# Kernel tuning notes

Hardware: AMD Instinct MI355X
Metric: run time of the kernel (lower is better)

## Reference

```python
import jax, jax.numpy as jnp
import numpy as np
import math

B, T, C = 8, 1024, 1024
H = 16
D = C // H
TI = 256
FF = 4 * C
EPS = 1e-5


def _ln(x, g, b):
    mu = jnp.mean(x, axis=-1, keepdims=True)
    var = jnp.mean(jnp.square(x - mu), axis=-1, keepdims=True)
    return (x - mu) * jax.lax.rsqrt(var + EPS) * g + b


def _gelu_tanh(x):
    return jax.nn.gelu(x, approximate=True)


def setup_inputs() -> dict:
    key = jax.random.key(0)
    ks = jax.random.split(key, 16)
    s = 0.02
    inp = {
        'x': jax.random.normal(ks[0], (B, T, C), jnp.float32),
        'x_img_feats': jax.random.normal(ks[1], (B, TI, C), jnp.float32),
        'ln1_g': jnp.ones((C,), jnp.float32), 'ln1_b': jnp.zeros((C,), jnp.float32),
        'ln2_g': jnp.ones((C,), jnp.float32), 'ln2_b': jnp.zeros((C,), jnp.float32),
        'W_attn': jax.random.normal(ks[2], (C, 3 * C), jnp.float32) * s,
        'b_attn': jnp.zeros((3 * C,), jnp.float32),
        'W_aproj': jax.random.normal(ks[3], (C, C), jnp.float32) * s,
        'b_aproj': jnp.zeros((C,), jnp.float32),
        'Wq': jax.random.normal(ks[4], (C, C), jnp.float32) * s,
        'bq': jnp.zeros((C,), jnp.float32),
        'Wk': jax.random.normal(ks[5], (C, C), jnp.float32) * s,
        'bk': jnp.zeros((C,), jnp.float32),
        'Wv': jax.random.normal(ks[6], (C, C), jnp.float32) * s,
        'bv': jnp.zeros((C,), jnp.float32),
        'Wcproj': jax.random.normal(ks[7], (C, C), jnp.float32) * s,
        'bcproj': jnp.zeros((C,), jnp.float32),
        'W_fc': jax.random.normal(ks[8], (C, FF), jnp.float32) * s,
        'b_fc': jnp.zeros((FF,), jnp.float32),
        'W_mproj': jax.random.normal(ks[9], (FF, C), jnp.float32) * s,
        'b_mproj': jnp.zeros((C,), jnp.float32),
    }
    return inp


def _heads(t):
    # (B, S, C) -> (B, H, S, D)
    return t.reshape(t.shape[0], t.shape[1], H, D).transpose(0, 2, 1, 3)


def _merge(t):
    # (B, H, S, D) -> (B, S, C)
    return t.transpose(0, 2, 1, 3).reshape(t.shape[0], t.shape[2], C)


def reference(x, x_img_feats, ln1_g, ln1_b, ln2_g, ln2_b,
              W_attn, b_attn, W_aproj, b_aproj,
              Wq, bq, Wk, bk, Wv, bv, Wcproj, bcproj,
              W_fc, b_fc, W_mproj, b_mproj):
    scale = 1.0 / math.sqrt(D)

    # causal self-attention
    h = _ln(x, ln1_g, ln1_b)
    qkv = h @ W_attn + b_attn
    q, k, v = jnp.split(qkv, 3, axis=-1)
    q, k, v = _heads(q), _heads(k), _heads(v)
    att = jnp.einsum('bhtd,bhsd->bhts', q, k) * scale
    causal = jnp.tril(jnp.ones((T, T), bool))
    att = jnp.where(causal[None, None], att, -jnp.inf)
    att = jax.nn.softmax(att, axis=-1)
    sa = _merge(jnp.einsum('bhts,bhsd->bhtd', att, v)) @ W_aproj + b_aproj
    x = x + sa

    # cross-attention (text queries, image keys/values)
    ht = _ln(x, ln1_g, ln1_b)
    q = _heads(ht @ Wq + bq)
    k = _heads(x_img_feats @ Wk + bk)
    v = _heads(x_img_feats @ Wv + bv)
    catt = jax.nn.softmax(jnp.einsum('bhtd,bhsd->bhts', q, k) * scale, axis=-1)
    ca = _merge(jnp.einsum('bhts,bhsd->bhtd', catt, v)) @ Wcproj + bcproj
    x = x + ca

    # MLP
    h2 = _ln(x, ln2_g, ln2_b)
    x = x + _gelu_tanh(h2 @ W_fc + b_fc) @ W_mproj + b_mproj
    return x
```

## Files before the change

kernel.cpp:

```cpp
#include <hip/hip_runtime.h>

#define B_ 8
#define T_ 1024
#define C_ 1024
#define H_ 16
#define D_ 64
#define TI_ 256
#define FF_ 4096
#define BT_ (B_*T_)
#define BTI_ (B_*TI_)

typedef __bf16 bf16x8 __attribute__((ext_vector_type(8)));
typedef float f32x4 __attribute__((ext_vector_type(4)));
typedef float f32x16 __attribute__((ext_vector_type(16)));

__device__ __forceinline__ unsigned short f2bf(float f){
  unsigned u = __float_as_uint(f);
  u += 0x7fffu + ((u>>16)&1u);
  return (unsigned short)(u>>16);
}

__device__ __forceinline__ void cp16(const void* g, void* l){
  __builtin_amdgcn_global_load_lds(
      (const __attribute__((address_space(1))) unsigned int*)(unsigned long long)g,
      (__attribute__((address_space(3))) unsigned int*)(unsigned long long)l,
      16, 0, 0);
}

__global__ __launch_bounds__(256) void gemm_bt(
    const unsigned short* __restrict__ A,
    const unsigned short* __restrict__ Bt,
    const float* __restrict__ bias,
    const float* __restrict__ resid,
    void* __restrict__ outp,
    int M, int N, int K, int mode)
{
  __shared__ unsigned short sA[128*64];
  __shared__ unsigned short sB[128*64];
  const int tid  = threadIdx.x;
  const int wid  = tid >> 6;
  const int lane = tid & 63;
  const int l32  = lane & 31;
  const int khalf = lane >> 5;

  int lin = blockIdx.y * gridDim.x + blockIdx.x;
  int nb  = gridDim.x * gridDim.y;
  if ((nb & 7) == 0){
    int per = nb >> 3;
    lin = (lin >> 3) + (lin & 7) * per;
  }
  const int bx = lin % gridDim.x;
  const int by = lin / gridDim.x;
  const int row0 = by * 128;
  const int col0 = bx * 128;
  const int wr = (wid >> 1) * 64;
  const int wc = (wid & 1) * 64;

  f32x16 acc[2][2];
#pragma unroll
  for (int i=0;i<2;i++)
#pragma unroll
    for (int j=0;j<2;j++)
#pragma unroll
      for (int r=0;r<16;r++) acc[i][j][r] = 0.f;

  for (int k0 = 0; k0 < K; k0 += 64){
    if (k0) __syncthreads();
#pragma unroll
    for (int r=0;r<8;r++){
      int chunk = wid*8 + r;
      int cA = chunk & 15;
      int slot = cA*64 + lane;
      int row = slot >> 3;
      int cc = (slot & 7) ^ (row & 7);
      if (chunk < 16)
        cp16(A  + (size_t)(row0+row)*K + (k0 + cc*8), sA + cA*512);
      else
        cp16(Bt + (size_t)(col0+row)*K + (k0 + cc*8), sB + cA*512);
    }
    __syncthreads();
    const char* sAb = (const char*)sA;
    const char* sBb = (const char*)sB;
#pragma unroll
    for (int kk=0;kk<4;kk++){
      bf16x8 af[2], bfb[2];
#pragma unroll
      for (int i=0;i<2;i++){
        int rr = wr + i*32 + l32;
        af[i] = *(const bf16x8*)(sAb + rr*128 + ((((kk<<1)+khalf) ^ (rr&7))<<4));
      }
#pragma unroll
      for (int j=0;j<2;j++){
        int rr = wc + j*32 + l32;
        bfb[j] = *(const bf16x8*)(sBb + rr*128 + ((((kk<<1)+khalf) ^ (rr&7))<<4));
      }
#pragma unroll
      for (int i=0;i<2;i++)
#pragma unroll
        for (int j=0;j<2;j++)
          acc[i][j] = __builtin_amdgcn_mfma_f32_32x32x16_bf16(af[i], bfb[j], acc[i][j], 0, 0, 0);
    }
  }

#pragma unroll
  for (int j=0;j<2;j++){
    int gc = col0 + wc + j*32 + l32;
    float bz = bias[gc];
#pragma unroll
    for (int i=0;i<2;i++){
      int gr_base = row0 + wr + i*32 + 4*khalf;
#pragma unroll
      for (int reg=0; reg<16; ++reg){
        int gr = gr_base + (reg&3) + 8*(reg>>2);
        float v = acc[i][j][reg] + bz;
        size_t idx = (size_t)gr*N + gc;
        if (mode == 0){
          ((unsigned short*)outp)[idx] = f2bf(v);
        } else if (mode == 1){
          float w = 1.5957691216057308f*(v + 0.044715f*v*v*v);
          float g = v / (1.f + __expf(-w));
          ((unsigned short*)outp)[idx] = f2bf(g);
        } else {
          ((float*)outp)[idx] = resid[idx] + v;
        }
      }
    }
  }
}

__global__ __launch_bounds__(256) void ln_fwd(
    const float* __restrict__ x, const float* __restrict__ g,
    const float* __restrict__ b, unsigned short* __restrict__ out)
{
  int row = blockIdx.x, t = threadIdx.x;
  const float4* xv = (const float4*)(x + (size_t)row*C_);
  float4 v = xv[t];
  float s  = v.x+v.y+v.z+v.w;
  float ss = v.x*v.x + v.y*v.y + v.z*v.z + v.w*v.w;
#pragma unroll
  for (int o=32;o>0;o>>=1){ s += __shfl_down(s,o); ss += __shfl_down(ss,o); }
  __shared__ float red[16];
  int wid = t>>6, lane = t&63;
  if (lane==0){ red[wid]=s; red[8+wid]=ss; }
  __syncthreads();
  if (t==0){
    red[0] = red[0]+red[1]+red[2]+red[3];
    red[8] = red[8]+red[9]+red[10]+red[11];
  }
  __syncthreads();
  float mu  = red[0] * (1.f/C_);
  float var = red[8] * (1.f/C_) - mu*mu;
  float rstd = rsqrtf(var + 1e-5f);
  float4 gv = ((const float4*)g)[t];
  float4 bv = ((const float4*)b)[t];
  ushort4 o;
  o.x = f2bf((v.x-mu)*rstd*gv.x + bv.x);
  o.y = f2bf((v.y-mu)*rstd*gv.y + bv.y);
  o.z = f2bf((v.z-mu)*rstd*gv.z + bv.z);
  o.w = f2bf((v.w-mu)*rstd*gv.w + bv.w);
  ((ushort4*)(out + (size_t)row*C_))[t] = o;
}

__global__ void wconv_t(const float* __restrict__ W, unsigned short* __restrict__ Wt,
                        int Kd, int Nd)
{
  __shared__ float tile[32][33];
  int tx = threadIdx.x, ty = threadIdx.y;
  int n0 = blockIdx.x*32, k0 = blockIdx.y*32;
#pragma unroll
  for (int j=0;j<4;j++)
    tile[ty+8*j][tx] = W[(size_t)(k0+ty+8*j)*Nd + (n0+tx)];
  __syncthreads();
#pragma unroll
  for (int j=0;j<4;j++)
    Wt[(size_t)(n0+ty+8*j)*Kd + (k0+tx)] = f2bf(tile[tx][ty+8*j]);
}

__global__ void conv_bf16(const float* __restrict__ X, unsigned short* __restrict__ Y, int n4)
{
  int i = blockIdx.x*256 + threadIdx.x;
  if (i < n4){
    float4 v = ((const float4*)X)[i];
    ushort4 o; o.x=f2bf(v.x); o.y=f2bf(v.y); o.z=f2bf(v.z); o.w=f2bf(v.w);
    ((ushort4*)Y)[i] = o;
  }
}

__global__ __launch_bounds__(256) void attn_fwd(
    const unsigned short* __restrict__ Q, int ldq,
    const unsigned short* __restrict__ Kp, const unsigned short* __restrict__ Vp, int ldkv,
    int kvT, int Skv, int Tq, int causal,
    unsigned short* __restrict__ Out, int ldo, float scale)
{
  __shared__ unsigned short sK[64*64];
  __shared__ unsigned short sV[64*64];
  __shared__ unsigned short sP[4*16*64];
  const int tid = threadIdx.x;
  const int wid = tid >> 6;
  const int lane = tid & 63;
  const int quad = lane >> 4;
  const int l16 = lane & 15;
  const int qt = blockIdx.x, h = blockIdx.y, b = blockIdx.z;
  const int hoff = h * D_;

  const int qrow = qt*64 + wid*16 + l16;
  const unsigned short* qb = Q + (size_t)(b*Tq + qrow)*ldq + hoff;
  bf16x8 qf[2];
  qf[0] = *(const bf16x8*)(qb + quad*8);
  qf[1] = *(const bf16x8*)(qb + 32 + quad*8);

  f32x4 zero = {0.f,0.f,0.f,0.f};
  f32x4 O[4];
#pragma unroll
  for (int j=0;j<4;j++) O[j] = zero;
  float mrun[4], lrun[4];
#pragma unroll
  for (int r=0;r<4;r++){ mrun[r] = -1e30f; lrun[r] = 0.f; }

  const int nkb = causal ? (qt+1) : ((Skv+63)>>6);
  char* sPw = (char*)sP + wid*2048;

  for (int kb=0; kb<nkb; ++kb){
    if (kb) __syncthreads();
#pragma unroll
    for (int ss=0; ss<2; ++ss){
      int slot = tid + ss*256;
      int srow = slot >> 3;
      int cc = (slot & 7) ^ (srow & 7);
      const unsigned short* g = Kp + (size_t)(b*kvT + kb*64 + srow)*ldkv + hoff + cc*8;
      *(uint4*)((char*)sK + slot*16) = *(const uint4*)g;
    }
    {
      int s_ = lane;
      int dbase = wid*16;
      const unsigned short* gv = Vp + (size_t)(b*kvT + kb*64 + s_)*ldkv + hoff + dbase;
      unsigned short vals[16];
      *(uint4*)(vals)   = *(const uint4*)(gv);
      *(uint4*)(vals+8) = *(const uint4*)(gv+8);
      int chunk = s_ >> 3;
      int sb = (s_ & 7)*2;
#pragma unroll
      for (int jj=0; jj<16; ++jj){
        int d = dbase + jj;
        *(unsigned short*)((char*)sV + d*128 + ((chunk ^ (d&7))<<4) + sb) = vals[jj];
      }
    }
    __syncthreads();

    f32x4 sacc[4];
#pragma unroll
    for (int j=0;j<4;j++) sacc[j] = zero;
#pragma unroll
    for (int j=0;j<4;j++){
      int krow = j*16 + l16;
#pragma unroll
      for (int kk=0;kk<2;kk++){
        bf16x8 kf = *(const bf16x8*)((const char*)sK + krow*128 + (((kk*4+quad) ^ (krow&7))<<4));
        sacc[j] = __builtin_amdgcn_mfma_f32_16x16x32_bf16(qf[kk], kf, sacc[j], 0, 0, 0);
      }
    }
    const int qa0 = qt*64 + wid*16 + quad*4;
    float sc[4][4];
#pragma unroll
    for (int j=0;j<4;j++){
      int key = kb*64 + j*16 + l16;
#pragma unroll
      for (int r=0;r<4;r++){
        float v = sacc[j][r] * scale;
        if (causal && key > qa0 + r) v = -1e30f;
        sc[j][r] = v;
      }
    }
    float mnew[4], alpha[4], rs[4];
#pragma unroll
    for (int r=0;r<4;r++){
      float m = fmaxf(fmaxf(sc[0][r], sc[1][r]), fmaxf(sc[2][r], sc[3][r]));
#pragma unroll
      for (int msk=1; msk<16; msk<<=1) m = fmaxf(m, __shfl_xor(m, msk));
      mnew[r] = fmaxf(mrun[r], m);
      alpha[r] = __expf(mrun[r] - mnew[r]);
      mrun[r] = mnew[r];
      rs[r] = 0.f;
    }
#pragma unroll
    for (int j=0;j<4;j++){
#pragma unroll
      for (int r=0;r<4;r++){
        float p = __expf(sc[j][r] - mnew[r]);
        rs[r] += p;
        int prow = quad*4 + r;
        int cole = j*16 + l16;
        *(unsigned short*)(sPw + prow*128 + (((cole>>3) ^ (prow&7))<<4) + (cole&7)*2) = f2bf(p);
      }
    }
#pragma unroll
    for (int r=0;r<4;r++){
#pragma unroll
      for (int msk=1; msk<16; msk<<=1) rs[r] += __shfl_xor(rs[r], msk);
      lrun[r] = lrun[r]*alpha[r] + rs[r];
    }
#pragma unroll
    for (int j=0;j<4;j++){
      O[j][0] *= alpha[0]; O[j][1] *= alpha[1];
      O[j][2] *= alpha[2]; O[j][3] *= alpha[3];
    }
    bf16x8 pf[2];
#pragma unroll
    for (int kk=0;kk<2;kk++)
      pf[kk] = *(const bf16x8*)(sPw + l16*128 + (((kk*4+quad) ^ (l16&7))<<4));
#pragma unroll
    for (int j=0;j<4;j++){
      int vrow = j*16 + l16;
#pragma unroll
      for (int kk=0;kk<2;kk++){
        bf16x8 vf = *(const bf16x8*)((const char*)sV + vrow*128 + (((kk*4+quad) ^ (vrow&7))<<4));
        O[j] = __builtin_amdgcn_mfma_f32_16x16x32_bf16(pf[kk], vf, O[j], 0, 0, 0);
      }
    }
  }
#pragma unroll
  for (int j=0;j<4;j++){
#pragma unroll
    for (int r=0;r<4;r++){
      int qa = qt*64 + wid*16 + quad*4 + r;
      float o = O[j][r] / lrun[r];
      Out[(size_t)(b*Tq + qa)*ldo + hoff + j*16 + l16] = f2bf(o);
    }
  }
}

extern "C" void kernel_launch(void* const* d_in, const int* in_sizes, int n_in,
                              void* d_out, int out_size, void* d_ws, size_t ws_size,
                              hipStream_t stream)
{
  const float* x       = (const float*)d_in[0];
  const float* ximg    = (const float*)d_in[1];
  const float* ln1_g   = (const float*)d_in[2];
  const float* ln1_b   = (const float*)d_in[3];
  const float* ln2_g   = (const float*)d_in[4];
  const float* ln2_b   = (const float*)d_in[5];
  const float* W_attn  = (const float*)d_in[6];
  const float* b_attn  = (const float*)d_in[7];
  const float* W_aproj = (const float*)d_in[8];
  const float* b_aproj = (const float*)d_in[9];
  const float* Wq = (const float*)d_in[10];
  const float* bq = (const float*)d_in[11];
  const float* Wk = (const float*)d_in[12];
  const float* bk = (const float*)d_in[13];
  const float* Wv = (const float*)d_in[14];
  const float* bv = (const float*)d_in[15];
  const float* Wcproj  = (const float*)d_in[16];
  const float* bcproj  = (const float*)d_in[17];
  const float* W_fc    = (const float*)d_in[18];
  const float* b_fc    = (const float*)d_in[19];
  const float* W_mproj = (const float*)d_in[20];
  const float* b_mproj = (const float*)d_in[21];

  char* ws = (char*)d_ws;
  unsigned short* wt_attn  = (unsigned short*)(ws + 0);
  unsigned short* wt_aproj = (unsigned short*)(ws + 6291456);
  unsigned short* wt_q     = (unsigned short*)(ws + 8388608);
  unsigned short* wt_k     = (unsigned short*)(ws + 10485760);
  unsigned short* wt_v     = (unsigned short*)(ws + 12582912);
  unsigned short* wt_cproj = (unsigned short*)(ws + 14680064);
  unsigned short* wt_fc    = (unsigned short*)(ws + 16777216);
  unsigned short* wt_mproj = (unsigned short*)(ws + 25165824);
  unsigned short* ximg_bf  = (unsigned short*)(ws + 33554432);
  float*          xcur     = (float*)(ws + 37748736);
  unsigned short* h_bf     = (unsigned short*)(ws + 71303168);
  unsigned short* qkv      = (unsigned short*)(ws + 88080384);
  unsigned short* att_out  = (unsigned short*)(ws + 88080384 + 50331648);
  unsigned short* u_bf     = (unsigned short*)(ws + 88080384);
  unsigned short* q2   = (unsigned short*)(ws + 155189248);
  unsigned short* k2v2 = (unsigned short*)(ws + 171966464);
  unsigned short* ca   = (unsigned short*)(ws + 180355072);
  float*          bkv  = (float*)(ws + 197132288);

  dim3 tb(32,8);
  wconv_t<<<dim3(96,32),  tb, 0, stream>>>(W_attn,  wt_attn,  1024, 3072);
  wconv_t<<<dim3(32,32),  tb, 0, stream>>>(W_aproj, wt_aproj, 1024, 1024);
  wconv_t<<<dim3(32,32),  tb, 0, stream>>>(Wq,      wt_q,     1024, 1024);
  wconv_t<<<dim3(32,32),  tb, 0, stream>>>(Wk,      wt_k,     1024, 1024);
  wconv_t<<<dim3(32,32),  tb, 0, stream>>>(Wv,      wt_v,     1024, 1024);
  wconv_t<<<dim3(32,32),  tb, 0, stream>>>(Wcproj,  wt_cproj, 1024, 1024);
  wconv_t<<<dim3(128,32), tb, 0, stream>>>(W_fc,    wt_fc,    1024, 4096);
  wconv_t<<<dim3(32,128), tb, 0, stream>>>(W_mproj, wt_mproj, 4096, 1024);
  conv_bf16<<<BTI_*C_/4/256, 256, 0, stream>>>(ximg, ximg_bf, BTI_*C_/4);
  hipMemcpyAsync(xcur, x, (size_t)BT_*C_*4, hipMemcpyDeviceToDevice, stream);
  hipMemcpyAsync(bkv,        bk, 4096, hipMemcpyDeviceToDevice, stream);
  hipMemcpyAsync(bkv + 1024, bv, 4096, hipMemcpyDeviceToDevice, stream);

  ln_fwd<<<BT_, 256, 0, stream>>>(x, ln1_g, ln1_b, h_bf);
  gemm_bt<<<dim3(24,64), 256, 0, stream>>>(h_bf, wt_attn, b_attn, nullptr, qkv, BT_, 3072, 1024, 0);
  attn_fwd<<<dim3(16,H_,B_), 256, 0, stream>>>(qkv, 3072, qkv+1024, qkv+2048, 3072,
                                               T_, T_, T_, 1, att_out, C_, 0.125f);
  gemm_bt<<<dim3(8,64), 256, 0, stream>>>(att_out, wt_aproj, b_aproj, xcur, xcur, BT_, 1024, 1024, 2);

  ln_fwd<<<BT_, 256, 0, stream>>>(xcur, ln1_g, ln1_b, h_bf);
  gemm_bt<<<dim3(8,64), 256, 0, stream>>>(h_bf, wt_q, bq, nullptr, q2, BT_, 1024, 1024, 0);
  gemm_bt<<<dim3(16,16), 256, 0, stream>>>(ximg_bf, wt_k, bkv, nullptr, k2v2, BTI_, 2048, 1024, 0);
  attn_fwd<<<dim3(16,H_,B_), 256, 0, stream>>>(q2, 1024, k2v2, k2v2+1024, 2048,
                                               TI_, TI_, T_, 0, ca, C_, 0.125f);
  gemm_bt<<<dim3(8,64), 256, 0, stream>>>(ca, wt_cproj, bcproj, xcur, xcur, BT_, 1024, 1024, 2);

  ln_fwd<<<BT_, 256, 0, stream>>>(xcur, ln2_g, ln2_b, h_bf);
  gemm_bt<<<dim3(32,64), 256, 0, stream>>>(h_bf, wt_fc, b_fc, nullptr, u_bf, BT_, 4096, 1024, 1);
  gemm_bt<<<dim3(8,64), 256, 0, stream>>>(u_bf, wt_mproj, b_mproj, xcur, (float*)d_out, BT_, 1024, 4096, 2);
}
```

Before: 839.2 us.

## Double-buffer attention K/V tiles, process two query tiles per block, batch weight conversions

The attention kernel now handles 128 query rows per block as two 64-row sub-tiles that share each loaded K/V tile, halving K/V traffic per query. It double-buffers K (via async global-to-LDS copies) and V (via register prefetch) so loads overlap the MFMA work. It also schedules heavy causal tiles first, folds the softmax scale into exp2, and sets a 3-blocks-per-CU launch bound. Separately, the five 1024x1024 weight conversions are merged into one launch, and the GEMM's XCD-aware block remapping is removed, which may hurt L2 locality on the GEMMs.

```diff
diff --git a/kernel.cpp b/kernel.cpp
--- a/kernel.cpp
+++ b/kernel.cpp
@@ -43,16 +43,8 @@
   const int l32  = lane & 31;
   const int khalf = lane >> 5;
 
-  int lin = blockIdx.y * gridDim.x + blockIdx.x;
-  int nb  = gridDim.x * gridDim.y;
-  if ((nb & 7) == 0){
-    int per = nb >> 3;
-    lin = (lin >> 3) + (lin & 7) * per;
-  }
-  const int bx = lin % gridDim.x;
-  const int by = lin / gridDim.x;
-  const int row0 = by * 128;
-  const int col0 = bx * 128;
+  const int row0 = blockIdx.y * 128;
+  const int col0 = blockIdx.x * 128;
   const int wr = (wid >> 1) * 64;
   const int wc = (wid & 1) * 64;
 
@@ -176,6 +168,27 @@
     Wt[(size_t)(n0+ty+8*j)*Kd + (k0+tx)] = f2bf(tile[tx][ty+8*j]);
 }
 
+__global__ void wconv_t5(const float* W0, const float* W1, const float* W2,
+                         const float* W3, const float* W4,
+                         unsigned short* O0, unsigned short* O1, unsigned short* O2,
+                         unsigned short* O3, unsigned short* O4)
+{
+  __shared__ float tile[32][33];
+  const float* Ws[5] = {W0,W1,W2,W3,W4};
+  unsigned short* Os[5] = {O0,O1,O2,O3,O4};
+  const float* W = Ws[blockIdx.z];
+  unsigned short* Wt = Os[blockIdx.z];
+  int tx = threadIdx.x, ty = threadIdx.y;
+  int n0 = blockIdx.x*32, k0 = blockIdx.y*32;
+#pragma unroll
+  for (int j=0;j<4;j++)
+    tile[ty+8*j][tx] = W[(size_t)(k0+ty+8*j)*1024 + (n0+tx)];
+  __syncthreads();
+#pragma unroll
+  for (int j=0;j<4;j++)
+    Wt[(size_t)(n0+ty+8*j)*1024 + (k0+tx)] = f2bf(tile[tx][ty+8*j]);
+}
+
 __global__ void conv_bf16(const float* __restrict__ X, unsigned short* __restrict__ Y, int n4)
 {
   int i = blockIdx.x*256 + threadIdx.x;
@@ -186,145 +199,193 @@
   }
 }
 
-__global__ __launch_bounds__(256) void attn_fwd(
+__global__ __launch_bounds__(256,3) void attn_fwd(
     const unsigned short* __restrict__ Q, int ldq,
     const unsigned short* __restrict__ Kp, const unsigned short* __restrict__ Vp, int ldkv,
     int kvT, int Skv, int Tq, int causal,
     unsigned short* __restrict__ Out, int ldo, float scale)
 {
-  __shared__ unsigned short sK[64*64];
-  __shared__ unsigned short sV[64*64];
-  __shared__ unsigned short sP[4*16*64];
+  __shared__ unsigned short sK[2][64*64];
+  __shared__ unsigned short sVT[2][64*64];
+  __shared__ unsigned short sP[8*16*64];
   const int tid = threadIdx.x;
   const int wid = tid >> 6;
   const int lane = tid & 63;
   const int quad = lane >> 4;
   const int l16 = lane & 15;
-  const int qt = blockIdx.x, h = blockIdx.y, b = blockIdx.z;
+  const int qt = gridDim.x - 1 - blockIdx.x;
+  const int h = blockIdx.y, b = blockIdx.z;
   const int hoff = h * D_;
-
-  const int qrow = qt*64 + wid*16 + l16;
-  const unsigned short* qb = Q + (size_t)(b*Tq + qrow)*ldq + hoff;
-  bf16x8 qf[2];
-  qf[0] = *(const bf16x8*)(qb + quad*8);
-  qf[1] = *(const bf16x8*)(qb + 32 + quad*8);
-
-  f32x4 zero = {0.f,0.f,0.f,0.f};
-  f32x4 O[4];
-#pragma unroll
-  for (int j=0;j<4;j++) O[j] = zero;
-  float mrun[4], lrun[4];
-#pragma unroll
-  for (int r=0;r<4;r++){ mrun[r] = -1e30f; lrun[r] = 0.f; }
-
-  const int nkb = causal ? (qt+1) : ((Skv+63)>>6);
-  char* sPw = (char*)sP + wid*2048;
-
-  for (int kb=0; kb<nkb; ++kb){
-    if (kb) __syncthreads();
+  const float c2 = scale * 1.4426950408889634f;
+
+  bf16x8 qf[2][2];
+#pragma unroll
+  for (int s=0;s<2;s++){
+    int qrow = qt*128 + s*64 + wid*16 + l16;
+    const unsigned short* qb = Q + (size_t)(b*Tq + qrow)*ldq + hoff;
+    qf[s][0] = *(const bf16x8*)(qb + quad*8);
+    qf[s][1] = *(const bf16x8*)(qb + 32 + quad*8);
+  }
+
+  f32x4 O[2][4];
+#pragma unroll
+  for (int s=0;s<2;s++)
+#pragma unroll
+    for (int j=0;j<4;j++) O[s][j] = (f32x4){0.f,0.f,0.f,0.f};
+  float mrun[2][4], lrun[2][4];
+#pragma unroll
+  for (int s=0;s<2;s++)
+#pragma unroll
+    for (int r=0;r<4;r++){ mrun[s][r] = -1e30f; lrun[s][r] = 0.f; }
+
+  const int nkb = causal ? (2*qt + 2) : ((Skv + 63) >> 6);
+
+  uint4 vreg0, vreg1;
+  const int vsrow = lane;
+  const int vdbase = wid*16;
+
+  {
+    const unsigned short* gv = Vp + (size_t)(b*kvT + vsrow)*ldkv + hoff + vdbase;
+    vreg0 = *(const uint4*)gv; vreg1 = *(const uint4*)(gv+8);
 #pragma unroll
     for (int ss=0; ss<2; ++ss){
       int slot = tid + ss*256;
       int srow = slot >> 3;
       int cc = (slot & 7) ^ (srow & 7);
-      const unsigned short* g = Kp + (size_t)(b*kvT + kb*64 + srow)*ldkv + hoff + cc*8;
-      *(uint4*)((char*)sK + slot*16) = *(const uint4*)g;
-    }
-    {
-      int s_ = lane;
-      int dbase = wid*16;
-      const unsigned short* gv = Vp + (size_t)(b*kvT + kb*64 + s_)*ldkv + hoff + dbase;
+      cp16(Kp + (size_t)(b*kvT + srow)*ldkv + hoff + cc*8,
+           sK[0] + (size_t)(wid*64 + ss*256)*8);
+    }
+    unsigned short vals[16];
+    *(uint4*)vals = vreg0; *(uint4*)(vals+8) = vreg1;
+    int chunk = vsrow >> 3, sb = (vsrow & 7)*2;
+#pragma unroll
+    for (int jj=0; jj<16; ++jj){
+      int d = vdbase + jj;
+      *(unsigned short*)((char*)sVT[0] + d*128 + ((chunk ^ (d&7))<<4) + sb) = vals[jj];
+    }
+  }
+  __syncthreads();
+
+  int cur = 0;
+  for (int kb=0; kb<nkb; ++kb){
+    const bool pre = (kb+1 < nkb);
+    if (pre){
+      const unsigned short* gv = Vp + (size_t)(b*kvT + (kb+1)*64 + vsrow)*ldkv + hoff + vdbase;
+      vreg0 = *(const uint4*)gv; vreg1 = *(const uint4*)(gv+8);
+#pragma unroll
+      for (int ss=0; ss<2; ++ss){
+        int slot = tid + ss*256;
+        int srow = slot >> 3;
+        int cc = (slot & 7) ^ (srow & 7);
+        cp16(Kp + (size_t)(b*kvT + (kb+1)*64 + srow)*ldkv + hoff + cc*8,
+             sK[cur^1] + (size_t)(wid*64 + ss*256)*8);
+      }
+    }
+    const char* sKb = (const char*)sK[cur];
+    const char* sVb = (const char*)sVT[cur];
+
+#pragma unroll
+    for (int s=0; s<2; ++s){
+      const int qb0 = qt*128 + s*64;
+      if (causal && kb*64 > qb0 + 63) continue;
+
+      f32x4 sacc[4];
+#pragma unroll
+      for (int j=0;j<4;j++) sacc[j] = (f32x4){0.f,0.f,0.f,0.f};
+#pragma unroll
+      for (int j=0;j<4;j++){
+        int krow = j*16 + l16;
+#pragma unroll
+        for (int kk=0;kk<2;kk++){
+          bf16x8 kf = *(const bf16x8*)(sKb + krow*128 + (((kk*4+quad) ^ (krow&7))<<4));
+          sacc[j] = __builtin_amdgcn_mfma_f32_16x16x32_bf16(qf[s][kk], kf, sacc[j], 0, 0, 0);
+        }
+      }
+      const int qa0 = qb0 + wid*16 + quad*4;
+      float sc[4][4];
+#pragma unroll
+      for (int j=0;j<4;j++){
+        int key = kb*64 + j*16 + l16;
+#pragma unroll
+        for (int r=0;r<4;r++){
+          float v = sacc[j][r];
+          if (causal && key > qa0 + r) v = -1e30f;
+          sc[j][r] = v;
+        }
+      }
+      float mnew[4], alpha[4], rs[4];
+#pragma unroll
+      for (int r=0;r<4;r++){
+        float m = fmaxf(fmaxf(sc[0][r], sc[1][r]), fmaxf(sc[2][r], sc[3][r]));
+#pragma unroll
+        for (int msk=1; msk<16; msk<<=1) m = fmaxf(m, __shfl_xor(m, msk));
+        mnew[r] = fmaxf(mrun[s][r], m);
+        alpha[r] = exp2f((mrun[s][r] - mnew[r]) * c2);
+        mrun[s][r] = mnew[r];
+        rs[r] = 0.f;
+      }
+      char* sPw = (char*)sP + (wid*2 + s)*2048;
+#pragma unroll
+      for (int j=0;j<4;j++){
+#pragma unroll
+        for (int r=0;r<4;r++){
+          float p = exp2f((sc[j][r] - mnew[r]) * c2);
+          rs[r] += p;
+          int prow = quad*4 + r;
+          int cole = j*16 + l16;
+          *(unsigned short*)(sPw + prow*128 + (((cole>>3) ^ (prow&7))<<4) + (cole&7)*2) = f2bf(p);
+        }
+      }
+#pragma unroll
+      for (int r=0;r<4;r++){
+#pragma unroll
+        for (int msk=1; msk<16; msk<<=1) rs[r] += __shfl_xor(rs[r], msk);
+        lrun[s][r] = lrun[s][r]*alpha[r] + rs[r];
+      }
+#pragma unroll
+      for (int j=0;j<4;j++){
+        O[s][j][0] *= alpha[0]; O[s][j][1] *= alpha[1];
+        O[s][j][2] *= alpha[2]; O[s][j][3] *= alpha[3];
+      }
+      bf16x8 pf[2];
+#pragma unroll
+      for (int kk=0;kk<2;kk++)
+        pf[kk] = *(const bf16x8*)(sPw + l16*128 + (((kk*4+quad) ^ (l16&7))<<4));
+#pragma unroll
+      for (int j=0;j<4;j++){
+        int vrow = j*16 + l16;
+#pragma unroll
+        for (int kk=0;kk<2;kk++){
+          bf16x8 vf = *(const bf16x8*)(sVb + vrow*128 + (((kk*4+quad) ^ (vrow&7))<<4));
+          O[s][j] = __builtin_amdgcn_mfma_f32_16x16x32_bf16(pf[kk], vf, O[s][j], 0, 0, 0);
+        }
+      }
+    }
+
+    if (pre){
       unsigned short vals[16];
-      *(uint4*)(vals)   = *(const uint4*)(gv);
-      *(uint4*)(vals+8) = *(const uint4*)(gv+8);
-      int chunk = s_ >> 3;
-      int sb = (s_ & 7)*2;
+      *(uint4*)vals = vreg0; *(uint4*)(vals+8) = vreg1;
+      int chunk = vsrow >> 3, sb = (vsrow & 7)*2;
 #pragma unroll
       for (int jj=0; jj<16; ++jj){
-        int d = dbase + jj;
-        *(unsigned short*)((char*)sV + d*128 + ((chunk ^ (d&7))<<4) + sb) = vals[jj];
+        int d = vdbase + jj;
+        *(unsigned short*)((char*)sVT[cur^1] + d*128 + ((chunk ^ (d&7))<<4) + sb) = vals[jj];
       }
     }
     __syncthreads();
-
-    f32x4 sacc[4];
-#pragma unroll
-    for (int j=0;j<4;j++) sacc[j] = zero;
+    cur ^= 1;
+  }
+
+#pragma unroll
+  for (int s=0;s<2;s++){
 #pragma unroll
     for (int j=0;j<4;j++){
-      int krow = j*16 + l16;
-#pragma unroll
-      for (int kk=0;kk<2;kk++){
-        bf16x8 kf = *(const bf16x8*)((const char*)sK + krow*128 + (((kk*4+quad) ^ (krow&7))<<4));
-        sacc[j] = __builtin_amdgcn_mfma_f32_16x16x32_bf16(qf[kk], kf, sacc[j], 0, 0, 0);
-      }
-    }
-    const int qa0 = qt*64 + wid*16 + quad*4;
-    float sc[4][4];
-#pragma unroll
-    for (int j=0;j<4;j++){
-      int key = kb*64 + j*16 + l16;
 #pragma unroll
       for (int r=0;r<4;r++){
-        float v = sacc[j][r] * scale;
-        if (causal && key > qa0 + r) v = -1e30f;
-        sc[j][r] = v;
-      }
-    }
-    float mnew[4], alpha[4], rs[4];
-#pragma unroll
-    for (int r=0;r<4;r++){
-      float m = fmaxf(fmaxf(sc[0][r], sc[1][r]), fmaxf(sc[2][r], sc[3][r]));
-#pragma unroll
-      for (int msk=1; msk<16; msk<<=1) m = fmaxf(m, __shfl_xor(m, msk));
-      mnew[r] = fmaxf(mrun[r], m);
-      alpha[r] = __expf(mrun[r] - mnew[r]);
-      mrun[r] = mnew[r];
-      rs[r] = 0.f;
-    }
-#pragma unroll
-    for (int j=0;j<4;j++){
-#pragma unroll
-      for (int r=0;r<4;r++){
-        float p = __expf(sc[j][r] - mnew[r]);
-        rs[r] += p;
-        int prow = quad*4 + r;
-        int cole = j*16 + l16;
-        *(unsigned short*)(sPw + prow*128 + (((cole>>3) ^ (prow&7))<<4) + (cole&7)*2) = f2bf(p);
-      }
-    }
-#pragma unroll
-    for (int r=0;r<4;r++){
-#pragma unroll
-      for (int msk=1; msk<16; msk<<=1) rs[r] += __shfl_xor(rs[r], msk);
-      lrun[r] = lrun[r]*alpha[r] + rs[r];
-    }
-#pragma unroll
-    for (int j=0;j<4;j++){
-      O[j][0] *= alpha[0]; O[j][1] *= alpha[1];
-      O[j][2] *= alpha[2]; O[j][3] *= alpha[3];
-    }
-    bf16x8 pf[2];
-#pragma unroll
-    for (int kk=0;kk<2;kk++)
-      pf[kk] = *(const bf16x8*)(sPw + l16*128 + (((kk*4+quad) ^ (l16&7))<<4));
-#pragma unroll
-    for (int j=0;j<4;j++){
-      int vrow = j*16 + l16;
-#pragma unroll
-      for (int kk=0;kk<2;kk++){
-        bf16x8 vf = *(const bf16x8*)((const char*)sV + vrow*128 + (((kk*4+quad) ^ (vrow&7))<<4));
-        O[j] = __builtin_amdgcn_mfma_f32_16x16x32_bf16(pf[kk], vf, O[j], 0, 0, 0);
-      }
-    }
-  }
-#pragma unroll
-  for (int j=0;j<4;j++){
-#pragma unroll
-    for (int r=0;r<4;r++){
-      int qa = qt*64 + wid*16 + quad*4 + r;
-      float o = O[j][r] / lrun[r];
-      Out[(size_t)(b*Tq + qa)*ldo + hoff + j*16 + l16] = f2bf(o);
+        int qa = qt*128 + s*64 + wid*16 + quad*4 + r;
+        float o = O[s][j][r] / lrun[s][r];
+        Out[(size_t)(b*Tq + qa)*ldo + hoff + j*16 + l16] = f2bf(o);
+      }
     }
   }
 }
@@ -377,12 +438,9 @@
   float*          bkv  = (float*)(ws + 197132288);
 
   dim3 tb(32,8);
+  wconv_t5<<<dim3(32,32,5), tb, 0, stream>>>(W_aproj, Wq, Wk, Wv, Wcproj,
+                                             wt_aproj, wt_q, wt_k, wt_v, wt_cproj);
   wconv_t<<<dim3(96,32),  tb, 0, stream>>>(W_attn,  wt_attn,  1024, 3072);
-  wconv_t<<<dim3(32,32),  tb, 0, stream>>>(W_aproj, wt_aproj, 1024, 1024);
-  wconv_t<<<dim3(32,32),  tb, 0, stream>>>(Wq,      wt_q,     1024, 1024);
-  wconv_t<<<dim3(32,32),  tb, 0, stream>>>(Wk,      wt_k,     1024, 1024);
-  wconv_t<<<dim3(32,32),  tb, 0, stream>>>(Wv,      wt_v,     1024, 1024);
-  wconv_t<<<dim3(32,32),  tb, 0, stream>>>(Wcproj,  wt_cproj, 1024, 1024);
   wconv_t<<<dim3(128,32), tb, 0, stream>>>(W_fc,    wt_fc,    1024, 4096);
   wconv_t<<<dim3(32,128), tb, 0, stream>>>(W_mproj, wt_mproj, 4096, 1024);
   conv_bf16<<<BTI_*C_/4/256, 256, 0, stream>>>(ximg, ximg_bf, BTI_*C_/4);
@@ -392,15 +450,15 @@
 
   ln_fwd<<<BT_, 256, 0, stream>>>(x, ln1_g, ln1_b, h_bf);
   gemm_bt<<<dim3(24,64), 256, 0, stream>>>(h_bf, wt_attn, b_attn, nullptr, qkv, BT_, 3072, 1024, 0);
-  attn_fwd<<<dim3(16,H_,B_), 256, 0, stream>>>(qkv, 3072, qkv+1024, qkv+2048, 3072,
-                                               T_, T_, T_, 1, att_out, C_, 0.125f);
+  attn_fwd<<<dim3(8,H_,B_), 256, 0, stream>>>(qkv, 3072, qkv+1024, qkv+2048, 3072,
+                                              T_, T_, T_, 1, att_out, C_, 0.125f);
   gemm_bt<<<dim3(8,64), 256, 0, stream>>>(att_out, wt_aproj, b_aproj, xcur, xcur, BT_, 1024, 1024, 2);
 
   ln_fwd<<<BT_, 256, 0, stream>>>(xcur, ln1_g, ln1_b, h_bf);
   gemm_bt<<<dim3(8,64), 256, 0, stream>>>(h_bf, wt_q, bq, nullptr, q2, BT_, 1024, 1024, 0);
   gemm_bt<<<dim3(16,16), 256, 0, stream>>>(ximg_bf, wt_k, bkv, nullptr, k2v2, BTI_, 2048, 1024, 0);
-  attn_fwd<<<dim3(16,H_,B_), 256, 0, stream>>>(q2, 1024, k2v2, k2v2+1024, 2048,
-                                               TI_, TI_, T_, 0, ca, C_, 0.125f);
+  attn_fwd<<<dim3(8,H_,B_), 256, 0, stream>>>(q2, 1024, k2v2, k2v2+1024, 2048,
+                                              TI_, TI_, T_, 0, ca, C_, 0.125f);
   gemm_bt<<<dim3(8,64), 256, 0, stream>>>(ca, wt_cproj, bcproj, xcur, xcur, BT_, 1024, 1024, 2);
 
   ln_fwd<<<BT_, 256, 0, stream>>>(xcur, ln2_g, ln2_b, h_bf);
```

Result: slower. 885.3 us (+5.5%).

## Write Q/K/V in head-major layout and reorder attention blocks causal-heavy first

Applied to the files above, without the earlier changes.

The GEMM epilogue gains a mode that scatters Q/K/V outputs into a contiguous per-(batch, head) layout, so attention loads 64-wide rows from one dense region and can copy K tiles with direct global-to-LDS loads. Attention now runs on a 1D grid that schedules the longest causal query tiles first and groups heads, and it uses exp2 with the scale folded into a single constant. The GEMM drops its block-index swizzle, and five small weight conversions are merged into one launch. In exchange, the GEMM stores become scattered and GEMM cache locality may drop without the swizzle.

```diff
diff --git a/kernel.cpp b/kernel.cpp
--- a/kernel.cpp
+++ b/kernel.cpp
@@ -33,7 +33,7 @@
     const float* __restrict__ bias,
     const float* __restrict__ resid,
     void* __restrict__ outp,
-    int M, int N, int K, int mode)
+    int M, int N, int K, int mode, int nkind, int tshift)
 {
   __shared__ unsigned short sA[128*64];
   __shared__ unsigned short sB[128*64];
@@ -43,16 +43,8 @@
   const int l32  = lane & 31;
   const int khalf = lane >> 5;
 
-  int lin = blockIdx.y * gridDim.x + blockIdx.x;
-  int nb  = gridDim.x * gridDim.y;
-  if ((nb & 7) == 0){
-    int per = nb >> 3;
-    lin = (lin >> 3) + (lin & 7) * per;
-  }
-  const int bx = lin % gridDim.x;
-  const int by = lin / gridDim.x;
-  const int row0 = by * 128;
-  const int col0 = bx * 128;
+  const int row0 = blockIdx.y * 128;
+  const int col0 = blockIdx.x * 128;
   const int wr = (wid >> 1) * 64;
   const int wc = (wid & 1) * 64;
 
@@ -113,15 +105,24 @@
       for (int reg=0; reg<16; ++reg){
         int gr = gr_base + (reg&3) + 8*(reg>>2);
         float v = acc[i][j][reg] + bz;
-        size_t idx = (size_t)gr*N + gc;
         if (mode == 0){
-          ((unsigned short*)outp)[idx] = f2bf(v);
+          ((unsigned short*)outp)[(size_t)gr*N + gc] = f2bf(v);
         } else if (mode == 1){
           float w = 1.5957691216057308f*(v + 0.044715f*v*v*v);
           float g = v / (1.f + __expf(-w));
-          ((unsigned short*)outp)[idx] = f2bf(g);
+          ((unsigned short*)outp)[(size_t)gr*N + gc] = f2bf(g);
+        } else if (mode == 2){
+          size_t idx = (size_t)gr*N + gc;
+          ((float*)outp)[idx] = resid[idx] + v;
         } else {
-          ((float*)outp)[idx] = resid[idx] + v;
+          int kind = gc >> 10;
+          int hc = gc & 1023;
+          int hh = hc >> 6;
+          int d  = hc & 63;
+          int bb = gr >> tshift;
+          int tt = gr & ((1<<tshift)-1);
+          size_t oidx = ((((size_t)(bb*16 + hh)*nkind + kind) << tshift) + tt)*64 + d;
+          ((unsigned short*)outp)[oidx] = f2bf(v);
         }
       }
     }
@@ -176,6 +177,27 @@
     Wt[(size_t)(n0+ty+8*j)*Kd + (k0+tx)] = f2bf(tile[tx][ty+8*j]);
 }
 
+__global__ void wconv_t5(const float* W0, const float* W1, const float* W2,
+                         const float* W3, const float* W4,
+                         unsigned short* O0, unsigned short* O1, unsigned short* O2,
+                         unsigned short* O3, unsigned short* O4)
+{
+  __shared__ float tile[32][33];
+  const float* Ws[5] = {W0,W1,W2,W3,W4};
+  unsigned short* Os[5] = {O0,O1,O2,O3,O4};
+  const float* W = Ws[blockIdx.z];
+  unsigned short* Wt = Os[blockIdx.z];
+  int tx = threadIdx.x, ty = threadIdx.y;
+  int n0 = blockIdx.x*32, k0 = blockIdx.y*32;
+#pragma unroll
+  for (int j=0;j<4;j++)
+    tile[ty+8*j][tx] = W[(size_t)(k0+ty+8*j)*1024 + (n0+tx)];
+  __syncthreads();
+#pragma unroll
+  for (int j=0;j<4;j++)
+    Wt[(size_t)(n0+ty+8*j)*1024 + (k0+tx)] = f2bf(tile[tx][ty+8*j]);
+}
+
 __global__ void conv_bf16(const float* __restrict__ X, unsigned short* __restrict__ Y, int n4)
 {
   int i = blockIdx.x*256 + threadIdx.x;
@@ -187,10 +209,10 @@
 }
 
 __global__ __launch_bounds__(256) void attn_fwd(
-    const unsigned short* __restrict__ Q, int ldq,
-    const unsigned short* __restrict__ Kp, const unsigned short* __restrict__ Vp, int ldkv,
-    int kvT, int Skv, int Tq, int causal,
-    unsigned short* __restrict__ Out, int ldo, float scale)
+    const unsigned short* __restrict__ Qb, unsigned int sQ,
+    const unsigned short* __restrict__ Kb, const unsigned short* __restrict__ Vb,
+    unsigned int sKV, int causal, int nkb_in,
+    unsigned short* __restrict__ Out, float scale)
 {
   __shared__ unsigned short sK[64*64];
   __shared__ unsigned short sV[64*64];
@@ -200,11 +222,19 @@
   const int lane = tid & 63;
   const int quad = lane >> 4;
   const int l16 = lane & 15;
-  const int qt = blockIdx.x, h = blockIdx.y, b = blockIdx.z;
-  const int hoff = h * D_;
+
+  const int L = blockIdx.x;
+  const int g  = (L & 7) + (L >> 7) * 8;
+  const int qt = 15 - ((L >> 3) & 15);
+  const int b = g >> 4, h = g & 15;
+  const float c2 = scale * 1.4426950408889634f;
+
+  const unsigned short* Qp = Qb + (size_t)g * sQ;
+  const unsigned short* Kp = Kb + (size_t)g * sKV;
+  const unsigned short* Vp = Vb + (size_t)g * sKV;
 
   const int qrow = qt*64 + wid*16 + l16;
-  const unsigned short* qb = Q + (size_t)(b*Tq + qrow)*ldq + hoff;
+  const unsigned short* qb = Qp + (size_t)qrow*64;
   bf16x8 qf[2];
   qf[0] = *(const bf16x8*)(qb + quad*8);
   qf[1] = *(const bf16x8*)(qb + 32 + quad*8);
@@ -217,7 +247,7 @@
 #pragma unroll
   for (int r=0;r<4;r++){ mrun[r] = -1e30f; lrun[r] = 0.f; }
 
-  const int nkb = causal ? (qt+1) : ((Skv+63)>>6);
+  const int nkb = causal ? (qt+1) : nkb_in;
   char* sPw = (char*)sP + wid*2048;
 
   for (int kb=0; kb<nkb; ++kb){
@@ -227,13 +257,12 @@
       int slot = tid + ss*256;
       int srow = slot >> 3;
       int cc = (slot & 7) ^ (srow & 7);
-      const unsigned short* g = Kp + (size_t)(b*kvT + kb*64 + srow)*ldkv + hoff + cc*8;
-      *(uint4*)((char*)sK + slot*16) = *(const uint4*)g;
+      cp16(Kp + (size_t)kb*4096 + srow*64 + cc*8, sK + (size_t)(wid*64 + ss*256)*8);
     }
     {
       int s_ = lane;
       int dbase = wid*16;
-      const unsigned short* gv = Vp + (size_t)(b*kvT + kb*64 + s_)*ldkv + hoff + dbase;
+      const unsigned short* gv = Vp + (size_t)kb*4096 + s_*64 + dbase;
       unsigned short vals[16];
       *(uint4*)(vals)   = *(const uint4*)(gv);
       *(uint4*)(vals+8) = *(const uint4*)(gv+8);
@@ -266,7 +295,7 @@
       int key = kb*64 + j*16 + l16;
 #pragma unroll
       for (int r=0;r<4;r++){
-        float v = sacc[j][r] * scale;
+        float v = sacc[j][r];
         if (causal && key > qa0 + r) v = -1e30f;
         sc[j][r] = v;
       }
@@ -278,7 +307,7 @@
 #pragma unroll
       for (int msk=1; msk<16; msk<<=1) m = fmaxf(m, __shfl_xor(m, msk));
       mnew[r] = fmaxf(mrun[r], m);
-      alpha[r] = __expf(mrun[r] - mnew[r]);
+      alpha[r] = exp2f((mrun[r] - mnew[r]) * c2);
       mrun[r] = mnew[r];
       rs[r] = 0.f;
     }
@@ -286,7 +315,7 @@
     for (int j=0;j<4;j++){
 #pragma unroll
       for (int r=0;r<4;r++){
-        float p = __expf(sc[j][r] - mnew[r]);
+        float p = exp2f((sc[j][r] - mnew[r]) * c2);
         rs[r] += p;
         int prow = quad*4 + r;
         int cole = j*16 + l16;
@@ -324,7 +353,7 @@
     for (int r=0;r<4;r++){
       int qa = qt*64 + wid*16 + quad*4 + r;
       float o = O[j][r] / lrun[r];
-      Out[(size_t)(b*Tq + qa)*ldo + hoff + j*16 + l16] = f2bf(o);
+      Out[(size_t)(b*T_ + qa)*C_ + h*64 + j*16 + l16] = f2bf(o);
     }
   }
 }
@@ -368,21 +397,18 @@
   unsigned short* ximg_bf  = (unsigned short*)(ws + 33554432);
   float*          xcur     = (float*)(ws + 37748736);
   unsigned short* h_bf     = (unsigned short*)(ws + 71303168);
-  unsigned short* qkv      = (unsigned short*)(ws + 88080384);
+  unsigned short* qkv_hm   = (unsigned short*)(ws + 88080384);
   unsigned short* att_out  = (unsigned short*)(ws + 88080384 + 50331648);
   unsigned short* u_bf     = (unsigned short*)(ws + 88080384);
-  unsigned short* q2   = (unsigned short*)(ws + 155189248);
-  unsigned short* k2v2 = (unsigned short*)(ws + 171966464);
-  unsigned short* ca   = (unsigned short*)(ws + 180355072);
-  float*          bkv  = (float*)(ws + 197132288);
+  unsigned short* q2_hm    = (unsigned short*)(ws + 155189248);
+  unsigned short* kv2_hm   = (unsigned short*)(ws + 171966464);
+  unsigned short* ca       = (unsigned short*)(ws + 180355072);
+  float*          bkv      = (float*)(ws + 197132288);
 
   dim3 tb(32,8);
+  wconv_t5<<<dim3(32,32,5), tb, 0, stream>>>(W_aproj, Wq, Wk, Wv, Wcproj,
+                                             wt_aproj, wt_q, wt_k, wt_v, wt_cproj);
   wconv_t<<<dim3(96,32),  tb, 0, stream>>>(W_attn,  wt_attn,  1024, 3072);
-  wconv_t<<<dim3(32,32),  tb, 0, stream>>>(W_aproj, wt_aproj, 1024, 1024);
-  wconv_t<<<dim3(32,32),  tb, 0, stream>>>(Wq,      wt_q,     1024, 1024);
-  wconv_t<<<dim3(32,32),  tb, 0, stream>>>(Wk,      wt_k,     1024, 1024);
-  wconv_t<<<dim3(32,32),  tb, 0, stream>>>(Wv,      wt_v,     1024, 1024);
-  wconv_t<<<dim3(32,32),  tb, 0, stream>>>(Wcproj,  wt_cproj, 1024, 1024);
   wconv_t<<<dim3(128,32), tb, 0, stream>>>(W_fc,    wt_fc,    1024, 4096);
   wconv_t<<<dim3(32,128), tb, 0, stream>>>(W_mproj, wt_mproj, 4096, 1024);
   conv_bf16<<<BTI_*C_/4/256, 256, 0, stream>>>(ximg, ximg_bf, BTI_*C_/4);
@@ -391,19 +417,26 @@
   hipMemcpyAsync(bkv + 1024, bv, 4096, hipMemcpyDeviceToDevice, stream);
 
   ln_fwd<<<BT_, 256, 0, stream>>>(x, ln1_g, ln1_b, h_bf);
-  gemm_bt<<<dim3(24,64), 256, 0, stream>>>(h_bf, wt_attn, b_attn, nullptr, qkv, BT_, 3072, 1024, 0);
-  attn_fwd<<<dim3(16,H_,B_), 256, 0, stream>>>(qkv, 3072, qkv+1024, qkv+2048, 3072,
-                                               T_, T_, T_, 1, att_out, C_, 0.125f);
-  gemm_bt<<<dim3(8,64), 256, 0, stream>>>(att_out, wt_aproj, b_aproj, xcur, xcur, BT_, 1024, 1024, 2);
+  gemm_bt<<<dim3(24,64), 256, 0, stream>>>(h_bf, wt_attn, b_attn, nullptr, qkv_hm,
+                                           BT_, 3072, 1024, 3, 3, 10);
+  attn_fwd<<<2048, 256, 0, stream>>>(qkv_hm, 3*T_*D_, qkv_hm + T_*D_, qkv_hm + 2*T_*D_,
+                                     3*T_*D_, 1, 16, att_out, 0.125f);
+  gemm_bt<<<dim3(8,64), 256, 0, stream>>>(att_out, wt_aproj, b_aproj, xcur, xcur,
+                                          BT_, 1024, 1024, 2, 0, 0);
 
   ln_fwd<<<BT_, 256, 0, stream>>>(xcur, ln1_g, ln1_b, h_bf);
-  gemm_bt<<<dim3(8,64), 256, 0, stream>>>(h_bf, wt_q, bq, nullptr, q2, BT_, 1024, 1024, 0);
-  gemm_bt<<<dim3(16,16), 256, 0, stream>>>(ximg_bf, wt_k, bkv, nullptr, k2v2, BTI_, 2048, 1024, 0);
-  attn_fwd<<<dim3(16,H_,B_), 256, 0, stream>>>(q2, 1024, k2v2, k2v2+1024, 2048,
-                                               TI_, TI_, T_, 0, ca, C_, 0.125f);
-  gemm_bt<<<dim3(8,64), 256, 0, stream>>>(ca, wt_cproj, bcproj, xcur, xcur, BT_, 1024, 1024, 2);
+  gemm_bt<<<dim3(8,64), 256, 0, stream>>>(h_bf, wt_q, bq, nullptr, q2_hm,
+                                          BT_, 1024, 1024, 3, 1, 10);
+  gemm_bt<<<dim3(16,16), 256, 0, stream>>>(ximg_bf, wt_k, bkv, nullptr, kv2_hm,
+                                           BTI_, 2048, 1024, 3, 2, 8);
+  attn_fwd<<<2048, 256, 0, stream>>>(q2_hm, T_*D_, kv2_hm, kv2_hm + TI_*D_,
+                                     2*TI_*D_, 0, 4, ca, 0.125f);
+  gemm_bt<<<dim3(8,64), 256, 0, stream>>>(ca, wt_cproj, bcproj, xcur, xcur,
+                                          BT_, 1024, 1024, 2, 0, 0);
 
   ln_fwd<<<BT_, 256, 0, stream>>>(xcur, ln2_g, ln2_b, h_bf);
-  gemm_bt<<<dim3(32,64), 256, 0, stream>>>(h_bf, wt_fc, b_fc, nullptr, u_bf, BT_, 4096, 1024, 1);
-  gemm_bt<<<dim3(8,64), 256, 0, stream>>>(u_bf, wt_mproj, b_mproj, xcur, (float*)d_out, BT_, 1024, 4096, 2);
-}
+  gemm_bt<<<dim3(32,64), 256, 0, stream>>>(h_bf, wt_fc, b_fc, nullptr, u_bf,
+                                           BT_, 4096, 1024, 1, 0, 0);
+  gemm_bt<<<dim3(8,64), 256, 0, stream>>>(u_bf, wt_mproj, b_mproj, xcur, (float*)d_out,
+                                          BT_, 1024, 4096, 2, 0, 0);
+}
```

Result: no change. 839.2 us (+0.0%).
